# Kernel optimization log

Hardware: AMD Instinct MI355X
Metric: run time of the kernel (lower is better)

Reference implementation:

```python
import jax, jax.numpy as jnp
import numpy as np

N = 100000   # nodes per branch
E = 1600000  # edges per branch
B = 512      # graphs in batch
D = 256      # input feature dim
C = 27       # number of side-effect labels
NEG_SLOPE = 0.2


def _gat_conv(x, src, dst, W, a_src, a_dst, b):
    """PyG GATConv, heads=1, with self loops. x:[N,din], src/dst:[E+N]."""
    n = x.shape[0]
    h = x @ W                               # [N, dout]
    al_s = h @ a_src                        # [N]
    al_d = h @ a_dst                        # [N]
    e = jax.nn.leaky_relu(al_s[src] + al_d[dst], NEG_SLOPE)  # [E+N]
    # segment softmax over destination nodes (self loops guarantee non-empty)
    m = jax.ops.segment_max(e, dst, num_segments=n)
    w = jnp.exp(e - m[dst])
    denom = jax.ops.segment_sum(w, dst, num_segments=n)
    alpha = w / denom[dst]                  # [E+N]
    out = jax.ops.segment_sum(h[src] * alpha[:, None], dst, num_segments=n)
    return out + b


def _with_self_loops(edge_index, n):
    loop = jnp.arange(n, dtype=edge_index.dtype)
    src = jnp.concatenate([edge_index[0], loop])
    dst = jnp.concatenate([edge_index[1], loop])
    return src, dst


def _mean_pool(x, batch, num_graphs):
    s = jax.ops.segment_sum(x, batch, num_segments=num_graphs)
    cnt = jax.ops.segment_sum(jnp.ones(x.shape[0], x.dtype), batch, num_segments=num_graphs)
    return s / jnp.maximum(cnt, 1.0)[:, None]


def _gat_params(key, din, dout):
    k = jax.random.split(key, 4)
    sc = 1.0 / np.sqrt(din)
    return (jax.random.normal(k[0], (din, dout), jnp.float32) * sc,
            jax.random.normal(k[1], (dout,), jnp.float32) * sc,
            jax.random.normal(k[2], (dout,), jnp.float32) * sc,
            jnp.zeros((dout,), jnp.float32))


def setup_inputs() -> dict:
    key = jax.random.key(0)
    ks = jax.random.split(key, 12)
    inp = {
        'x_s': jax.random.normal(ks[0], (N, D), jnp.float32),
        'x_t': jax.random.normal(ks[1], (N, D), jnp.float32),
        'edge_index_s': jax.random.randint(ks[2], (2, E), 0, N, jnp.int32),
        'edge_index_t': jax.random.randint(ks[3], (2, E), 0, N, jnp.int32),
        'xs_batch': jnp.sort(jax.random.randint(ks[4], (N,), 0, B, jnp.int32)),
        'xt_batch': jnp.sort(jax.random.randint(ks[5], (N,), 0, B, jnp.int32)),
    }
    for name, kk, din, dout in [('s1', ks[6], D, D // 2), ('s2', ks[7], D // 2, D // 4),
                                 ('t1', ks[8], D, D // 2), ('t2', ks[9], D // 2, D // 4)]:
        W, a_s, a_d, b = _gat_params(kk, din, dout)
        inp[f'W_{name}'] = W
        inp[f'a_src_{name}'] = a_s
        inp[f'a_dst_{name}'] = a_d
        inp[f'b_{name}'] = b
    inp['lin_w'] = jax.random.normal(ks[10], (D // 4, C), jnp.float32) / np.sqrt(D // 4)
    inp['lin_b'] = jnp.zeros((C,), jnp.float32)
    return inp


def reference(x_s, x_t,
              W_s1, a_src_s1, a_dst_s1, b_s1,
              W_s2, a_src_s2, a_dst_s2, b_s2,
              W_t1, a_src_t1, a_dst_t1, b_t1,
              W_t2, a_src_t2, a_dst_t2, b_t2,
              lin_w, lin_b,
              edge_index_s, edge_index_t, xs_batch, xt_batch):
    src_s, dst_s = _with_self_loops(edge_index_s, N)
    src_t, dst_t = _with_self_loops(edge_index_t, N)

    x1 = _gat_conv(x_s, src_s, dst_s, W_s1, a_src_s1, a_dst_s1, b_s1)
    x2 = _gat_conv(x1, src_s, dst_s, W_s2, a_src_s2, a_dst_s2, b_s2)
    xs = _mean_pool(x2, xs_batch, B)

    x3 = _gat_conv(x_t, src_t, dst_t, W_t1, a_src_t1, a_dst_t1, b_t1)
    x4 = _gat_conv(x3, src_t, dst_t, W_t2, a_src_t2, a_dst_t2, b_t2)
    xt = _mean_pool(x4, xt_batch, B)

    out = (xs + xt) @ lin_w + lin_b        # [B, C]
    return jax.nn.sigmoid(out)
```

## Files before the change

kernel.cpp:

```cpp
#include <hip/hip_runtime.h>
#include <hip/hip_bf16.h>
#include <math.h>

#define NEG_SLOPE 0.2f

static const int NN = 100000;
static const int EE = 1600000;
static const int BB = 512;
static const int NTOT = 2 * NN;
static const int ETOT = 2 * EE;
static const int NBUK = (NTOT + 511) / 512;
static const int CHUNK = 4096;
static const int NBLK = (ETOT + CHUNK - 1) / CHUNK;
static const int GB = (NN + 63) / 64;

typedef __attribute__((ext_vector_type(8))) short bf16x8;
typedef __attribute__((ext_vector_type(4))) float f32x4;

__device__ __forceinline__ float leaky(float x) { return x >= 0.f ? x : NEG_SLOPE * x; }

__device__ __forceinline__ unsigned short f2b(float f) {
    __hip_bfloat16 h = __float2bfloat16(f);
    return *reinterpret_cast<unsigned short*>(&h);
}
__device__ __forceinline__ float b2f_lo(unsigned v) { return __uint_as_float(v << 16); }
__device__ __forceinline__ float b2f_hi(unsigned v) { return __uint_as_float(v & 0xFFFF0000u); }
__device__ __forceinline__ unsigned packb(float a, float b) {
    return (unsigned)f2b(a) | ((unsigned)f2b(b) << 16);
}

__global__ void wt2_kernel(const float* __restrict__ Ws, const float* __restrict__ Wt_,
                           unsigned short* __restrict__ WT, int K, int N) {
    int idx = blockIdx.x * blockDim.x + threadIdx.x;
    if (idx >= 2 * K * N) return;
    int br = idx >= K * N;
    int j = idx - br * K * N;
    int n = j / K, k = j - n * K;
    const float* W = br ? Wt_ : Ws;
    WT[idx] = f2b(W[(size_t)k * N + n]);
}

template <int K, int N, bool ABF>
__global__ __launch_bounds__(256, 3) void gemm_fused_kernel(
        const void* __restrict__ Av_s, const void* __restrict__ Av_t,
        const unsigned short* __restrict__ WT,
        const float* __restrict__ as_s, const float* __restrict__ ad_s,
        const float* __restrict__ as_t, const float* __restrict__ ad_t,
        unsigned* __restrict__ hb, float* __restrict__ al_s, float* __restrict__ al_d,
        int nblk) {
    constexpr int NT2 = N / 32;
    __shared__ float als0[64], ald0[64];
    const int bid = blockIdx.x;
    const int br = (bid >= nblk) ? 1 : 0;
    const int lb = bid - br * nblk;
    const int t = threadIdx.x;
    const int l = t & 63, w = t >> 6;
    const int wm = w >> 1, wn = w & 1;
    const int rl = l & 15, kh = l >> 4;
    const int row0 = lb * 64 + wm * 32;
    const int r0 = min(row0 + rl, NN - 1);
    const int r1 = min(row0 + 16 + rl, NN - 1);
    const void* Av = br ? Av_t : Av_s;
    const unsigned short* WTb = WT + (size_t)br * N * K;
    const float* asv = br ? as_t : as_s;
    const float* adv = br ? ad_t : ad_s;

    f32x4 acc[2][NT2];
    #pragma unroll
    for (int g = 0; g < 2; g++)
        #pragma unroll
        for (int q = 0; q < NT2; q++) acc[g][q] = (f32x4){0.f, 0.f, 0.f, 0.f};

    #pragma unroll
    for (int k0 = 0; k0 < K; k0 += 32) {
        bf16x8 a0v, a1v;
        if constexpr (ABF) {
            const unsigned short* A = (const unsigned short*)Av;
            a0v = *(const bf16x8*)(A + (size_t)r0 * K + k0 + kh * 8);
            a1v = *(const bf16x8*)(A + (size_t)r1 * K + k0 + kh * 8);
        } else {
            const float* A = (const float*)Av;
            float4 x0 = *(const float4*)(A + (size_t)r0 * K + k0 + kh * 8);
            float4 x1 = *(const float4*)(A + (size_t)r0 * K + k0 + kh * 8 + 4);
            float4 y0 = *(const float4*)(A + (size_t)r1 * K + k0 + kh * 8);
            float4 y1 = *(const float4*)(A + (size_t)r1 * K + k0 + kh * 8 + 4);
            union { bf16x8 v; unsigned short u[8]; } au, bu;
            au.u[0] = f2b(x0.x); au.u[1] = f2b(x0.y); au.u[2] = f2b(x0.z); au.u[3] = f2b(x0.w);
            au.u[4] = f2b(x1.x); au.u[5] = f2b(x1.y); au.u[6] = f2b(x1.z); au.u[7] = f2b(x1.w);
            bu.u[0] = f2b(y0.x); bu.u[1] = f2b(y0.y); bu.u[2] = f2b(y0.z); bu.u[3] = f2b(y0.w);
            bu.u[4] = f2b(y1.x); bu.u[5] = f2b(y1.y); bu.u[6] = f2b(y1.z); bu.u[7] = f2b(y1.w);
            a0v = au.v; a1v = bu.v;
        }
        #pragma unroll
        for (int q = 0; q < NT2; q++) {
            int c = wn * (N / 2) + q * 16 + rl;
            bf16x8 bv = *(const bf16x8*)(WTb + (size_t)c * K + k0 + kh * 8);
            acc[0][q] = __builtin_amdgcn_mfma_f32_16x16x32_bf16(a0v, bv, acc[0][q], 0, 0, 0);
            acc[1][q] = __builtin_amdgcn_mfma_f32_16x16x32_bf16(a1v, bv, acc[1][q], 0, 0, 0);
        }
    }

    float asr[NT2], adr[NT2];
    #pragma unroll
    for (int q = 0; q < NT2; q++) {
        int c = wn * (N / 2) + q * 16 + rl;
        asr[q] = asv[c];
        adr[q] = adv[c];
    }

    float psA[2][4], pdA[2][4];
    #pragma unroll
    for (int rg = 0; rg < 2; rg++) {
        #pragma unroll
        for (int i = 0; i < 4; i++) {
            float ps = 0.f, pd = 0.f;
            #pragma unroll
            for (int q = 0; q < NT2; q++) {
                float v = acc[rg][q][i];
                ps += v * asr[q];
                pd += v * adr[q];
            }
            #pragma unroll
            for (int off = 1; off < 16; off <<= 1) {
                ps += __shfl_xor(ps, off);
                pd += __shfl_xor(pd, off);
            }
            psA[rg][i] = ps;
            pdA[rg][i] = pd;
        }
    }
    if (wn == 0 && rl == 0) {
        #pragma unroll
        for (int rg = 0; rg < 2; rg++)
            #pragma unroll
            for (int i = 0; i < 4; i++) {
                int rloc = wm * 32 + rg * 16 + kh * 4 + i;
                als0[rloc] = psA[rg][i];
                ald0[rloc] = pdA[rg][i];
            }
    }
    __syncthreads();
    if (wn == 1 && rl == 0) {
        #pragma unroll
        for (int rg = 0; rg < 2; rg++)
            #pragma unroll
            for (int i = 0; i < 4; i++) {
                int rloc = wm * 32 + rg * 16 + kh * 4 + i;
                int rlocal = lb * 64 + rloc;
                if (rlocal < NN) {
                    int g = br * NN + rlocal;
                    al_s[g] = psA[rg][i] + als0[rloc];
                    al_d[g] = pdA[rg][i] + ald0[rloc];
                }
            }
    }
    #pragma unroll
    for (int rg = 0; rg < 2; rg++) {
        #pragma unroll
        for (int i = 0; i < 4; i++) {
            int rlocal = lb * 64 + wm * 32 + rg * 16 + kh * 4 + i;
            bool ok = (rlocal < NN);
            int g = br * NN + rlocal;
            #pragma unroll
            for (int q = 0; q < NT2; q++) {
                float v = acc[rg][q][i];
                float hi = __shfl_xor(v, 1);
                if (ok && !(rl & 1)) {
                    int c = wn * (N / 2) + q * 16 + rl;
                    hb[(size_t)g * (N / 2) + (c >> 1)] = packb(v, hi);
                }
            }
        }
    }
}

__global__ __launch_bounds__(256) void bin_sort_kernel(const int* __restrict__ src_s,
                                                       const int* __restrict__ dst_s,
                                                       const int* __restrict__ src_t,
                                                       const int* __restrict__ dst_t,
                                                       uint2* __restrict__ region,
                                                       int* __restrict__ shist) {
    __shared__ int hist[512];
    __shared__ int part[256];
    __shared__ int cur[512];
    __shared__ uint2 lbuf[CHUNK];
    const int b = blockIdx.x, t = threadIdx.x;
    const int base = b * CHUNK;
    const int cnt = min(CHUNK, ETOT - base);
    hist[t] = 0; hist[t + 256] = 0;
    __syncthreads();
    unsigned es[16], ed[16];
    #pragma unroll
    for (int i = 0; i < 16; i++) {
        int li = i * 256 + t;
        if (li < cnt) {
            int e = base + li;
            if (e < EE) {
                es[i] = (unsigned)src_s[e];
                ed[i] = (unsigned)dst_s[e];
            } else {
                es[i] = (unsigned)src_t[e - EE] + NN;
                ed[i] = (unsigned)dst_t[e - EE] + NN;
            }
            atomicAdd(&hist[ed[i] >> 9], 1);
        }
    }
    __syncthreads();
    int d0 = hist[2 * t], d1 = hist[2 * t + 1];
    int s = d0 + d1;
    part[t] = s;
    __syncthreads();
    for (int off = 1; off < 256; off <<= 1) {
        int u = (t >= off) ? part[t - off] : 0;
        __syncthreads();
        part[t] += u;
        __syncthreads();
    }
    int ex = part[t] - s;
    cur[2 * t] = ex;
    cur[2 * t + 1] = ex + d0;
    if (2 * t < NBUK + 1) shist[(2 * t) * NBLK + b] = ex;
    if (2 * t + 1 < NBUK + 1) shist[(2 * t + 1) * NBLK + b] = ex + d0;
    __syncthreads();
    #pragma unroll
    for (int i = 0; i < 16; i++) {
        int li = i * 256 + t;
        if (li < cnt) {
            int slot = atomicAdd(&cur[ed[i] >> 9], 1);
            lbuf[slot] = make_uint2(es[i], ed[i]);
        }
    }
    __syncthreads();
    for (int i = t; i < cnt; i += 256) region[base + i] = lbuf[i];
}

__global__ void bucket_tot_kernel(const int* __restrict__ shist, int* __restrict__ btot) {
    __shared__ int red[256];
    const int k = blockIdx.x, t = threadIdx.x;
    int s = 0;
    for (int b = t; b < NBLK; b += 256)
        s += shist[(k + 1) * NBLK + b] - shist[k * NBLK + b];
    red[t] = s;
    __syncthreads();
    for (int off = 128; off > 0; off >>= 1) {
        if (t < off) red[t] += red[t + off];
        __syncthreads();
    }
    if (t == 0) btot[k] = red[0];
}

__global__ void bucket_scan_kernel(const int* __restrict__ btot, int* __restrict__ bbase) {
    __shared__ int part[256];
    int t = threadIdx.x;
    int v0 = (2 * t < NBUK) ? btot[2 * t] : 0;
    int v1 = (2 * t + 1 < NBUK) ? btot[2 * t + 1] : 0;
    int s = v0 + v1;
    part[t] = s;
    __syncthreads();
    for (int off = 1; off < 256; off <<= 1) {
        int u = (t >= off) ? part[t - off] : 0;
        __syncthreads();
        part[t] += u;
        __syncthreads();
    }
    int ex = part[t] - s;
    if (2 * t < NBUK) bbase[2 * t] = ex;
    if (2 * t + 1 < NBUK) bbase[2 * t + 1] = ex + v0;
}

__global__ __launch_bounds__(256) void csr_bucket_kernel(const uint2* __restrict__ region,
                                                         const int* __restrict__ shist,
                                                         const int* __restrict__ bbase,
                                                         int* __restrict__ rowptr,
                                                         int* __restrict__ col) {
    __shared__ int deg[512];
    __shared__ int part[256];
    __shared__ int cur[512];
    const int k = blockIdx.x, t = threadIdx.x;
    const int n0 = k * 512;
    const int nloc = min(512, NTOT - n0);
    const int base = bbase[k];
    deg[t] = 0; deg[t + 256] = 0;
    __syncthreads();
    for (int b = t; b < NBLK; b += 256) {
        int s0 = shist[k * NBLK + b], s1 = shist[(k + 1) * NBLK + b];
        for (int i = s0; i < s1; i++) {
            uint2 e = region[(size_t)b * CHUNK + i];
            atomicAdd(&deg[(int)e.y - n0], 1);
        }
    }
    __syncthreads();
    int d0 = deg[2 * t], d1 = deg[2 * t + 1];
    int s = d0 + d1;
    part[t] = s;
    __syncthreads();
    for (int off = 1; off < 256; off <<= 1) {
        int u = (t >= off) ? part[t - off] : 0;
        __syncthreads();
        part[t] += u;
        __syncthreads();
    }
    int ex = part[t] - s;
    cur[2 * t] = ex;
    cur[2 * t + 1] = ex + d0;
    if (2 * t < nloc) rowptr[n0 + 2 * t] = base + ex;
    if (2 * t + 1 < nloc) rowptr[n0 + 2 * t + 1] = base + ex + d0;
    if (t == 0 && n0 + nloc == NTOT) rowptr[NTOT] = base + part[255];
    __syncthreads();
    for (int b = t; b < NBLK; b += 256) {
        int s0 = shist[k * NBLK + b], s1 = shist[(k + 1) * NBLK + b];
        for (int i = s0; i < s1; i++) {
            uint2 e = region[(size_t)b * CHUNK + i];
            int pos = atomicAdd(&cur[(int)e.y - n0], 1);
            col[base + pos] = (int)e.x;
        }
    }
}

__global__ void brow2_kernel(const int* __restrict__ bs, const int* __restrict__ bt,
                             int* __restrict__ brow_s, int* __restrict__ brow_t) {
    int g = blockIdx.x * blockDim.x + threadIdx.x;
    const int* batch;
    int* brow;
    int gg;
    if (g <= BB) { batch = bs; brow = brow_s; gg = g; }
    else if (g <= 2 * BB + 1) { batch = bt; brow = brow_t; gg = g - (BB + 1); }
    else return;
    int lo = 0, hi = NN;
    while (lo < hi) {
        int mid = (lo + hi) >> 1;
        if (batch[mid] < gg) lo = mid + 1; else hi = mid;
    }
    brow[gg] = lo;
}

__global__ void gat_gather128_kernel(const int* __restrict__ rowptr, const int* __restrict__ col,
                                     const float* __restrict__ al_s, const float* __restrict__ al_d,
                                     const unsigned* __restrict__ hb,
                                     const float* __restrict__ bias_s,
                                     const float* __restrict__ bias_t,
                                     unsigned* __restrict__ outb) {
    int node = blockIdx.x * 4 + (threadIdx.x >> 6);
    int lane = threadIdx.x & 63;
    if (node >= NTOT) return;
    const float* bias = (node < NN) ? bias_s : bias_t;
    const int beg = rowptr[node], end = rowptr[node + 1];
    const float ald = al_d[node];
    const float e_self = leaky(al_s[node] + ald);

    float acc0 = 0.f, acc1 = 0.f, dsum = 0.f;
    for (int base = beg; base < end; base += 64) {
        int i = base + lane;
        float w = 0.f; int s = 0;
        if (i < end) {
            s = col[i];
            w = expf(leaky(al_s[s] + ald));
        }
        dsum += w;
        int cnt = min(64, end - base);
        int j = 0;
        for (; j + 8 <= cnt; j += 8) {
            float wj[8]; int sj[8];
            #pragma unroll
            for (int u = 0; u < 8; u++) { wj[u] = __shfl(w, j + u); sj[u] = __shfl(s, j + u); }
            unsigned v[8];
            #pragma unroll
            for (int u = 0; u < 8; u++) v[u] = hb[(size_t)sj[u] * 64 + lane];
            #pragma unroll
            for (int u = 0; u < 8; u++) {
                acc0 += wj[u] * b2f_lo(v[u]);
                acc1 += wj[u] * b2f_hi(v[u]);
            }
        }
        for (; j < cnt; j++) {
            float wj = __shfl(w, j);
            int sj = __shfl(s, j);
            unsigned v = hb[(size_t)sj * 64 + lane];
            acc0 += wj * b2f_lo(v);
            acc1 += wj * b2f_hi(v);
        }
    }
    #pragma unroll
    for (int off = 32; off > 0; off >>= 1) dsum += __shfl_xor(dsum, off);

    float wself = expf(e_self);
    dsum += wself;
    float inv = 1.f / dsum;
    unsigned sv = hb[(size_t)node * 64 + lane];
    int c0 = 2 * lane, c1 = c0 + 1;
    float o0 = bias[c0] + (acc0 + wself * b2f_lo(sv)) * inv;
    float o1 = bias[c1] + (acc1 + wself * b2f_hi(sv)) * inv;
    outb[(size_t)node * 64 + lane] = packb(o0, o1);
}

__global__ void gat_gather64_kernel(const int* __restrict__ rowptr, const int* __restrict__ col,
                                    const float* __restrict__ al_s, const float* __restrict__ al_d,
                                    const unsigned* __restrict__ hb,
                                    const float* __restrict__ bias_s,
                                    const float* __restrict__ bias_t,
                                    float* __restrict__ out) {
    int node = blockIdx.x * 4 + (threadIdx.x >> 6);
    int lane = threadIdx.x & 63;
    if (node >= NTOT) return;
    const float* bias = (node < NN) ? bias_s : bias_t;
    const int sl = lane & 31, half = lane >> 5;
    const int beg = rowptr[node], end = rowptr[node + 1];
    const float ald = al_d[node];
    const float e_self = leaky(al_s[node] + ald);

    float acc0 = 0.f, acc1 = 0.f, dsum = 0.f;
    for (int base = beg; base < end; base += 64) {
        int i = base + lane;
        float w = 0.f; int s = 0;
        if (i < end) {
            s = col[i];
            w = expf(leaky(al_s[s] + ald));
        }
        dsum += w;
        int cnt = min(64, end - base);
        int j = 0;
        for (; j + 8 <= cnt; j += 8) {
            float wj[4]; int sj[4];
            #pragma unroll
            for (int u = 0; u < 4; u++) {
                int idx = j + 2 * u + half;
                wj[u] = __shfl(w, idx);
                sj[u] = __shfl(s, idx);
            }
            unsigned v[4];
            #pragma unroll
            for (int u = 0; u < 4; u++) v[u] = hb[(size_t)sj[u] * 32 + sl];
            #pragma unroll
            for (int u = 0; u < 4; u++) {
                acc0 += wj[u] * b2f_lo(v[u]);
                acc1 += wj[u] * b2f_hi(v[u]);
            }
        }
        for (; j < cnt; j += 2) {
            int idx = j + half;
            float wj = (idx < cnt) ? __shfl(w, idx) : 0.f;
            int sj = __shfl(s, idx < cnt ? idx : 0);
            unsigned v = hb[(size_t)sj * 32 + sl];
            acc0 += wj * b2f_lo(v);
            acc1 += wj * b2f_hi(v);
        }
    }
    acc0 += __shfl_xor(acc0, 32);
    acc1 += __shfl_xor(acc1, 32);
    #pragma unroll
    for (int off = 32; off > 0; off >>= 1) dsum += __shfl_xor(dsum, off);

    float wself = expf(e_self);
    dsum += wself;
    float inv = 1.f / dsum;
    if (half == 0) {
        unsigned sv = hb[(size_t)node * 32 + sl];
        float* op = out + (size_t)node * 64;
        int c0 = 2 * sl;
        float o0 = bias[c0] + (acc0 + wself * b2f_lo(sv)) * inv;
        float o1 = bias[c0 + 1] + (acc1 + wself * b2f_hi(sv)) * inv;
        *(float2*)(op + c0) = make_float2(o0, o1);
    }
}

__global__ void pool_seg_kernel(const float* __restrict__ x,
                                const int* __restrict__ brow_s, const int* __restrict__ brow_t,
                                float* __restrict__ pooled_s, float* __restrict__ pooled_t) {
    __shared__ float red[4][64];
    int g = blockIdx.x;
    int tb = g >= BB;
    int gb = g - tb * BB;
    const int* brow = tb ? brow_t : brow_s;
    float* pooled = tb ? pooled_t : pooled_s;
    int off = tb ? NN : 0;
    int lane = threadIdx.x & 63, w = threadIdx.x >> 6;
    int beg = brow[gb], end = brow[gb + 1];
    float acc = 0.f;
    for (int n = beg + w; n < end; n += 4)
        acc += x[(size_t)(off + n) * 64 + lane];
    red[w][lane] = acc;
    __syncthreads();
    if (w == 0) {
        float s = red[0][lane] + red[1][lane] + red[2][lane] + red[3][lane];
        float cnt = (float)(end - beg);
        pooled[(size_t)gb * 64 + lane] = s / fmaxf(cnt, 1.f);
    }
}

__global__ void final_kernel(const float* __restrict__ ps, const float* __restrict__ pt,
                             const float* __restrict__ lw, const float* __restrict__ lb,
                             float* __restrict__ out) {
    int g = blockIdx.x;
    int c = threadIdx.x;
    if (c >= 27) return;
    float acc = lb[c];
    #pragma unroll 8
    for (int k = 0; k < 64; k++) {
        float xv = ps[g * 64 + k] + pt[g * 64 + k];
        acc += xv * lw[k * 27 + c];
    }
    out[g * 27 + c] = 1.f / (1.f + expf(-acc));
}

extern "C" void kernel_launch(void* const* d_in, const int* in_sizes, int n_in,
                              void* d_out, int out_size, void* d_ws, size_t ws_size,
                              hipStream_t stream) {
    const float* x_s = (const float*)d_in[0];
    const float* x_t = (const float*)d_in[1];
    const int* ei_s = (const int*)d_in[2];
    const int* ei_t = (const int*)d_in[3];
    const int* xs_batch = (const int*)d_in[4];
    const int* xt_batch = (const int*)d_in[5];
    const float* W_s1 = (const float*)d_in[6];
    const float* a_src_s1 = (const float*)d_in[7];
    const float* a_dst_s1 = (const float*)d_in[8];
    const float* b_s1 = (const float*)d_in[9];
    const float* W_s2 = (const float*)d_in[10];
    const float* a_src_s2 = (const float*)d_in[11];
    const float* a_dst_s2 = (const float*)d_in[12];
    const float* b_s2 = (const float*)d_in[13];
    const float* W_t1 = (const float*)d_in[14];
    const float* a_src_t1 = (const float*)d_in[15];
    const float* a_dst_t1 = (const float*)d_in[16];
    const float* b_t1 = (const float*)d_in[17];
    const float* W_t2 = (const float*)d_in[18];
    const float* a_src_t2 = (const float*)d_in[19];
    const float* a_dst_t2 = (const float*)d_in[20];
    const float* b_t2 = (const float*)d_in[21];
    const float* lin_w = (const float*)d_in[22];
    const float* lin_b = (const float*)d_in[23];
    float* out = (float*)d_out;

    unsigned* hb = (unsigned*)d_ws;
    uint2* region = (uint2*)d_ws;
    unsigned* out1b = hb + (size_t)NTOT * 64;
    float* out2 = (float*)out1b;
    int* col = (int*)(out1b + (size_t)NTOT * 64);
    float* al_s = (float*)(col + ETOT);
    float* al_d = al_s + NTOT;
    float* pooled_s = al_d + NTOT;
    float* pooled_t = pooled_s + (size_t)BB * 64;
    unsigned short* WT1 = (unsigned short*)(pooled_t + (size_t)BB * 64);
    unsigned short* WT2 = WT1 + 2 * 256 * 128;
    int* rowptr = (int*)(WT2 + 2 * 128 * 64);
    int* shist = rowptr + NTOT + 1;
    int* btot = shist + (NBUK + 1) * NBLK;
    int* bbase = btot + NBUK;
    int* brow_s = bbase + NBUK;
    int* brow_t = brow_s + BB + 1;

    const int* src_s = ei_s;
    const int* dst_s = ei_s + EE;
    const int* src_t = ei_t;
    const int* dst_t = ei_t + EE;

    bin_sort_kernel<<<NBLK, 256, 0, stream>>>(src_s, dst_s, src_t, dst_t, region, shist);
    bucket_tot_kernel<<<NBUK, 256, 0, stream>>>(shist, btot);
    bucket_scan_kernel<<<1, 256, 0, stream>>>(btot, bbase);
    csr_bucket_kernel<<<NBUK, 256, 0, stream>>>(region, shist, bbase, rowptr, col);

    wt2_kernel<<<(2 * 256 * 128 + 255) / 256, 256, 0, stream>>>(W_s1, W_t1, WT1, 256, 128);
    gemm_fused_kernel<256, 128, false><<<2 * GB, 256, 0, stream>>>(
        x_s, x_t, WT1, a_src_s1, a_dst_s1, a_src_t1, a_dst_t1, hb, al_s, al_d, GB);
    gat_gather128_kernel<<<(NTOT + 3) / 4, 256, 0, stream>>>(
        rowptr, col, al_s, al_d, hb, b_s1, b_t1, out1b);

    wt2_kernel<<<(2 * 128 * 64 + 255) / 256, 256, 0, stream>>>(W_s2, W_t2, WT2, 128, 64);
    gemm_fused_kernel<128, 64, true><<<2 * GB, 256, 0, stream>>>(
        out1b, (const unsigned short*)out1b + (size_t)NN * 128, WT2,
        a_src_s2, a_dst_s2, a_src_t2, a_dst_t2, hb, al_s, al_d, GB);
    gat_gather64_kernel<<<(NTOT + 3) / 4, 256, 0, stream>>>(
        rowptr, col, al_s, al_d, hb, b_s2, b_t2, out2);

    brow2_kernel<<<(2 * (BB + 1) + 255) / 256, 256, 0, stream>>>(xs_batch, xt_batch, brow_s, brow_t);
    pool_seg_kernel<<<2 * BB, 256, 0, stream>>>(out2, brow_s, brow_t, pooled_s, pooled_t);
    final_kernel<<<BB, 32, 0, stream>>>(pooled_s, pooled_t, lin_w, lin_b, out);
}
```

Before: 516.4 us.

## Gather four edges per wave step with wide vector loads; hoist GEMM A loads

The neighbour-aggregation kernels now split each wave into four 16-lane slots, each handling a different edge per step. Each slot reads a full feature row with 16-byte (128-wide) or 8-byte (64-wide) vector loads, and the partial sums are combined with cross-slot shuffles at the end. This replaces the scalar 4-byte per-lane loads and is meant to cut instruction count and issue more bytes per memory request. The projection GEMM also loads all A fragments for a K chunk before its MFMA loop, so more loads are in flight at once. The cost is higher register pressure, plus wasted loads of row 0 for padding edges when the edge count is not a multiple of four.

```diff
diff --git a/kernel.cpp b/kernel.cpp
--- a/kernel.cpp
+++ b/kernel.cpp
@@ -71,32 +71,55 @@
         #pragma unroll
         for (int q = 0; q < NT2; q++) acc[g][q] = (f32x4){0.f, 0.f, 0.f, 0.f};
 
-    #pragma unroll
-    for (int k0 = 0; k0 < K; k0 += 32) {
-        bf16x8 a0v, a1v;
-        if constexpr (ABF) {
-            const unsigned short* A = (const unsigned short*)Av;
-            a0v = *(const bf16x8*)(A + (size_t)r0 * K + k0 + kh * 8);
-            a1v = *(const bf16x8*)(A + (size_t)r1 * K + k0 + kh * 8);
-        } else {
-            const float* A = (const float*)Av;
-            float4 x0 = *(const float4*)(A + (size_t)r0 * K + k0 + kh * 8);
-            float4 x1 = *(const float4*)(A + (size_t)r0 * K + k0 + kh * 8 + 4);
-            float4 y0 = *(const float4*)(A + (size_t)r1 * K + k0 + kh * 8);
-            float4 y1 = *(const float4*)(A + (size_t)r1 * K + k0 + kh * 8 + 4);
-            union { bf16x8 v; unsigned short u[8]; } au, bu;
-            au.u[0] = f2b(x0.x); au.u[1] = f2b(x0.y); au.u[2] = f2b(x0.z); au.u[3] = f2b(x0.w);
-            au.u[4] = f2b(x1.x); au.u[5] = f2b(x1.y); au.u[6] = f2b(x1.z); au.u[7] = f2b(x1.w);
-            bu.u[0] = f2b(y0.x); bu.u[1] = f2b(y0.y); bu.u[2] = f2b(y0.z); bu.u[3] = f2b(y0.w);
-            bu.u[4] = f2b(y1.x); bu.u[5] = f2b(y1.y); bu.u[6] = f2b(y1.z); bu.u[7] = f2b(y1.w);
-            a0v = au.v; a1v = bu.v;
-        }
-        #pragma unroll
-        for (int q = 0; q < NT2; q++) {
-            int c = wn * (N / 2) + q * 16 + rl;
-            bf16x8 bv = *(const bf16x8*)(WTb + (size_t)c * K + k0 + kh * 8);
-            acc[0][q] = __builtin_amdgcn_mfma_f32_16x16x32_bf16(a0v, bv, acc[0][q], 0, 0, 0);
-            acc[1][q] = __builtin_amdgcn_mfma_f32_16x16x32_bf16(a1v, bv, acc[1][q], 0, 0, 0);
+    if constexpr (ABF) {
+        const unsigned short* A = (const unsigned short*)Av;
+        bf16x8 A0[4], A1[4];
+        #pragma unroll
+        for (int kb = 0; kb < 4; kb++) {
+            A0[kb] = *(const bf16x8*)(A + (size_t)r0 * K + kb * 32 + kh * 8);
+            A1[kb] = *(const bf16x8*)(A + (size_t)r1 * K + kb * 32 + kh * 8);
+        }
+        #pragma unroll
+        for (int kb = 0; kb < 4; kb++) {
+            #pragma unroll
+            for (int q = 0; q < NT2; q++) {
+                int c = wn * (N / 2) + q * 16 + rl;
+                bf16x8 bv = *(const bf16x8*)(WTb + (size_t)c * K + kb * 32 + kh * 8);
+                acc[0][q] = __builtin_amdgcn_mfma_f32_16x16x32_bf16(A0[kb], bv, acc[0][q], 0, 0, 0);
+                acc[1][q] = __builtin_amdgcn_mfma_f32_16x16x32_bf16(A1[kb], bv, acc[1][q], 0, 0, 0);
+            }
+        }
+    } else {
+        const float* A = (const float*)Av;
+        #pragma unroll
+        for (int kc = 0; kc < K; kc += 128) {
+            float4 A0[8], A1[8];
+            #pragma unroll
+            for (int kb = 0; kb < 4; kb++) {
+                const float* p0 = A + (size_t)r0 * K + kc + kb * 32 + kh * 8;
+                const float* p1 = A + (size_t)r1 * K + kc + kb * 32 + kh * 8;
+                A0[2 * kb] = *(const float4*)p0;
+                A0[2 * kb + 1] = *(const float4*)(p0 + 4);
+                A1[2 * kb] = *(const float4*)p1;
+                A1[2 * kb + 1] = *(const float4*)(p1 + 4);
+            }
+            #pragma unroll
+            for (int kb = 0; kb < 4; kb++) {
+                float4 x0 = A0[2 * kb], x1 = A0[2 * kb + 1];
+                float4 y0 = A1[2 * kb], y1 = A1[2 * kb + 1];
+                union { bf16x8 v; unsigned short u[8]; } au, bu;
+                au.u[0] = f2b(x0.x); au.u[1] = f2b(x0.y); au.u[2] = f2b(x0.z); au.u[3] = f2b(x0.w);
+                au.u[4] = f2b(x1.x); au.u[5] = f2b(x1.y); au.u[6] = f2b(x1.z); au.u[7] = f2b(x1.w);
+                bu.u[0] = f2b(y0.x); bu.u[1] = f2b(y0.y); bu.u[2] = f2b(y0.z); bu.u[3] = f2b(y0.w);
+                bu.u[4] = f2b(y1.x); bu.u[5] = f2b(y1.y); bu.u[6] = f2b(y1.z); bu.u[7] = f2b(y1.w);
+                #pragma unroll
+                for (int q = 0; q < NT2; q++) {
+                    int c = wn * (N / 2) + q * 16 + rl;
+                    bf16x8 bv = *(const bf16x8*)(WTb + (size_t)c * K + kc + kb * 32 + kh * 8);
+                    acc[0][q] = __builtin_amdgcn_mfma_f32_16x16x32_bf16(au.v, bv, acc[0][q], 0, 0, 0);
+                    acc[1][q] = __builtin_amdgcn_mfma_f32_16x16x32_bf16(bu.v, bv, acc[1][q], 0, 0, 0);
+                }
+            }
         }
     }
 
@@ -344,11 +367,13 @@
     int lane = threadIdx.x & 63;
     if (node >= NTOT) return;
     const float* bias = (node < NN) ? bias_s : bias_t;
+    const int slot = lane >> 4, sub = lane & 15;
     const int beg = rowptr[node], end = rowptr[node + 1];
     const float ald = al_d[node];
     const float e_self = leaky(al_s[node] + ald);
 
-    float acc0 = 0.f, acc1 = 0.f, dsum = 0.f;
+    float acc[8] = {};
+    float dsum = 0.f;
     for (int base = beg; base < end; base += 64) {
         int i = base + lane;
         float w = 0.f; int s = 0;
@@ -358,27 +383,21 @@
         }
         dsum += w;
         int cnt = min(64, end - base);
-        int j = 0;
-        for (; j + 8 <= cnt; j += 8) {
-            float wj[8]; int sj[8];
-            #pragma unroll
-            for (int u = 0; u < 8; u++) { wj[u] = __shfl(w, j + u); sj[u] = __shfl(s, j + u); }
-            unsigned v[8];
-            #pragma unroll
-            for (int u = 0; u < 8; u++) v[u] = hb[(size_t)sj[u] * 64 + lane];
-            #pragma unroll
-            for (int u = 0; u < 8; u++) {
-                acc0 += wj[u] * b2f_lo(v[u]);
-                acc1 += wj[u] * b2f_hi(v[u]);
-            }
-        }
-        for (; j < cnt; j++) {
-            float wj = __shfl(w, j);
-            int sj = __shfl(s, j);
-            unsigned v = hb[(size_t)sj * 64 + lane];
-            acc0 += wj * b2f_lo(v);
-            acc1 += wj * b2f_hi(v);
-        }
+        for (int j = 0; j < cnt; j += 4) {
+            int idx = j + slot;
+            float wj = __shfl(w, idx);
+            int sj = __shfl(s, idx);
+            uint4 v = *(const uint4*)(hb + (size_t)sj * 64 + sub * 4);
+            acc[0] += wj * b2f_lo(v.x); acc[1] += wj * b2f_hi(v.x);
+            acc[2] += wj * b2f_lo(v.y); acc[3] += wj * b2f_hi(v.y);
+            acc[4] += wj * b2f_lo(v.z); acc[5] += wj * b2f_hi(v.z);
+            acc[6] += wj * b2f_lo(v.w); acc[7] += wj * b2f_hi(v.w);
+        }
+    }
+    #pragma unroll
+    for (int k = 0; k < 8; k++) {
+        acc[k] += __shfl_xor(acc[k], 16);
+        acc[k] += __shfl_xor(acc[k], 32);
     }
     #pragma unroll
     for (int off = 32; off > 0; off >>= 1) dsum += __shfl_xor(dsum, off);
@@ -386,11 +405,18 @@
     float wself = expf(e_self);
     dsum += wself;
     float inv = 1.f / dsum;
-    unsigned sv = hb[(size_t)node * 64 + lane];
-    int c0 = 2 * lane, c1 = c0 + 1;
-    float o0 = bias[c0] + (acc0 + wself * b2f_lo(sv)) * inv;
-    float o1 = bias[c1] + (acc1 + wself * b2f_hi(sv)) * inv;
-    outb[(size_t)node * 64 + lane] = packb(o0, o1);
+    if (slot == 0) {
+        uint4 sv = *(const uint4*)(hb + (size_t)node * 64 + sub * 4);
+        float sf[8] = { b2f_lo(sv.x), b2f_hi(sv.x), b2f_lo(sv.y), b2f_hi(sv.y),
+                        b2f_lo(sv.z), b2f_hi(sv.z), b2f_lo(sv.w), b2f_hi(sv.w) };
+        float o[8];
+        #pragma unroll
+        for (int k = 0; k < 8; k++)
+            o[k] = bias[sub * 8 + k] + (acc[k] + wself * sf[k]) * inv;
+        uint4 r = make_uint4(packb(o[0], o[1]), packb(o[2], o[3]),
+                             packb(o[4], o[5]), packb(o[6], o[7]));
+        *(uint4*)(outb + (size_t)node * 64 + sub * 4) = r;
+    }
 }
 
 __global__ void gat_gather64_kernel(const int* __restrict__ rowptr, const int* __restrict__ col,
@@ -403,12 +429,13 @@
     int lane = threadIdx.x & 63;
     if (node >= NTOT) return;
     const float* bias = (node < NN) ? bias_s : bias_t;
-    const int sl = lane & 31, half = lane >> 5;
+    const int slot = lane >> 4, sub = lane & 15;
     const int beg = rowptr[node], end = rowptr[node + 1];
     const float ald = al_d[node];
     const float e_self = leaky(al_s[node] + ald);
 
-    float acc0 = 0.f, acc1 = 0.f, dsum = 0.f;
+    float acc[4] = {};
+    float dsum = 0.f;
     for (int base = beg; base < end; base += 64) {
         int i = base + lane;
         float w = 0.f; int s = 0;
@@ -418,48 +445,35 @@
         }
         dsum += w;
         int cnt = min(64, end - base);
-        int j = 0;
-        for (; j + 8 <= cnt; j += 8) {
-            float wj[4]; int sj[4];
-            #pragma unroll
-            for (int u = 0; u < 4; u++) {
-                int idx = j + 2 * u + half;
-                wj[u] = __shfl(w, idx);
-                sj[u] = __shfl(s, idx);
-            }
-            unsigned v[4];
-            #pragma unroll
-            for (int u = 0; u < 4; u++) v[u] = hb[(size_t)sj[u] * 32 + sl];
-            #pragma unroll
-            for (int u = 0; u < 4; u++) {
-                acc0 += wj[u] * b2f_lo(v[u]);
-                acc1 += wj[u] * b2f_hi(v[u]);
-            }
-        }
-        for (; j < cnt; j += 2) {
-            int idx = j + half;
-            float wj = (idx < cnt) ? __shfl(w, idx) : 0.f;
-            int sj = __shfl(s, idx < cnt ? idx : 0);
-            unsigned v = hb[(size_t)sj * 32 + sl];
-            acc0 += wj * b2f_lo(v);
-            acc1 += wj * b2f_hi(v);
-        }
-    }
-    acc0 += __shfl_xor(acc0, 32);
-    acc1 += __shfl_xor(acc1, 32);
+        for (int j = 0; j < cnt; j += 4) {
+            int idx = j + slot;
+            float wj = __shfl(w, idx);
+            int sj = __shfl(s, idx);
+            uint2 v = *(const uint2*)(hb + (size_t)sj * 32 + sub * 2);
+            acc[0] += wj * b2f_lo(v.x); acc[1] += wj * b2f_hi(v.x);
+            acc[2] += wj * b2f_lo(v.y); acc[3] += wj * b2f_hi(v.y);
+        }
+    }
+    #pragma unroll
+    for (int k = 0; k < 4; k++) {
+        acc[k] += __shfl_xor(acc[k], 16);
+        acc[k] += __shfl_xor(acc[k], 32);
+    }
     #pragma unroll
     for (int off = 32; off > 0; off >>= 1) dsum += __shfl_xor(dsum, off);
 
     float wself = expf(e_self);
     dsum += wself;
     float inv = 1.f / dsum;
-    if (half == 0) {
-        unsigned sv = hb[(size_t)node * 32 + sl];
-        float* op = out + (size_t)node * 64;
-        int c0 = 2 * sl;
-        float o0 = bias[c0] + (acc0 + wself * b2f_lo(sv)) * inv;
-        float o1 = bias[c0 + 1] + (acc1 + wself * b2f_hi(sv)) * inv;
-        *(float2*)(op + c0) = make_float2(o0, o1);
+    if (slot == 0) {
+        uint2 sv = *(const uint2*)(hb + (size_t)node * 32 + sub * 2);
+        float sf[4] = { b2f_lo(sv.x), b2f_hi(sv.x), b2f_lo(sv.y), b2f_hi(sv.y) };
+        float4 o;
+        o.x = bias[sub * 4 + 0] + (acc[0] + wself * sf[0]) * inv;
+        o.y = bias[sub * 4 + 1] + (acc[1] + wself * sf[1]) * inv;
+        o.z = bias[sub * 4 + 2] + (acc[2] + wself * sf[2]) * inv;
+        o.w = bias[sub * 4 + 3] + (acc[3] + wself * sf[3]) * inv;
+        *(float4*)(out + (size_t)node * 64 + sub * 4) = o;
     }
 }
 
```

After: 518.1 us. Within noise of the previous version (+0.3%).
